# Kernel optimization log

Hardware: AMD Instinct MI355X
Metric: run time of the kernel (lower is better)

## Reference

```python
import jax, jax.numpy as jnp
import numpy as np

D_MODEL = 1024
D_STATE = 16
D_CONV = 4
BATCH = 2
SEQ = 2048


def setup_inputs() -> dict:
    key = jax.random.key(0)
    ks = jax.random.split(key, 10)
    s = lambda fan_in: 1.0 / np.sqrt(fan_in)
    x = jax.random.normal(ks[0], (BATCH, SEQ, D_MODEL), dtype=jnp.float32)
    W_in = jax.random.normal(ks[1], (D_MODEL, 2 * D_MODEL), dtype=jnp.float32) * s(D_MODEL)
    conv_w = jax.random.normal(ks[2], (D_MODEL, D_CONV), dtype=jnp.float32) * s(D_CONV)
    conv_b = jax.random.normal(ks[3], (D_MODEL,), dtype=jnp.float32) * 0.01
    W_x = jax.random.normal(ks[4], (D_MODEL, 2 * D_STATE), dtype=jnp.float32) * s(D_MODEL)
    W_dt = jax.random.normal(ks[5], (D_MODEL, D_MODEL), dtype=jnp.float32) * s(D_MODEL)
    b_dt = jax.random.normal(ks[6], (D_MODEL,), dtype=jnp.float32) * 0.01
    A_log = jax.random.normal(ks[7], (D_MODEL,), dtype=jnp.float32) * 0.1
    D_param = jnp.ones((D_MODEL,), dtype=jnp.float32)
    W_out = jax.random.normal(ks[8], (D_MODEL, D_MODEL), dtype=jnp.float32) * s(D_MODEL)
    return {"x": x, "W_in": W_in, "conv_w": conv_w, "conv_b": conv_b,
            "W_x": W_x, "W_dt": W_dt, "b_dt": b_dt, "A_log": A_log,
            "D_param": D_param, "W_out": W_out}


def _selective_scan(x, A, dt, B, C):
    # x, dt: [b, l, d]; A: [d]; B, C: [b, l, n]
    b, l, d = x.shape
    n = B.shape[-1]
    h0 = jnp.zeros((b, d, n), dtype=x.dtype)

    def step(h, inp):
        x_t, dt_t, B_t, C_t = inp  # [b,d], [b,d], [b,n], [b,n]
        dA = jnp.exp(dt_t * A)[..., None]            # [b, d, 1]
        h = h * dA + x_t[..., None] * B_t[:, None, :]  # [b, d, n]
        y_t = jnp.einsum('bdn,bn->bd', h, C_t)
        return h, y_t

    xs = (jnp.swapaxes(x, 0, 1), jnp.swapaxes(dt, 0, 1),
          jnp.swapaxes(B, 0, 1), jnp.swapaxes(C, 0, 1))
    _, ys = jax.lax.scan(step, h0, xs)               # ys: [l, b, d]
    return jnp.swapaxes(ys, 0, 1)


def _forward(x, W_in, conv_w, conv_b, W_x, W_dt, b_dt, A_log, D_param, W_out):
    seq_len = x.shape[1]
    xz = x @ W_in                                     # [b, l, 2d]
    x_ssm, z = jnp.split(xz, 2, axis=-1)
    # causal depthwise conv (torch pads both sides then slices -> left pad only)
    xc = jnp.swapaxes(x_ssm, 1, 2)                    # [b, d, l]
    kernel = conv_w[:, None, :]                       # [d, 1, k]
    xc = jax.lax.conv_general_dilated(
        xc, kernel, window_strides=(1,), padding=[(D_CONV - 1, 0)],
        dimension_numbers=('NCH', 'OIH', 'NCH'), feature_group_count=D_MODEL)
    xc = xc + conv_b[None, :, None]
    x_ssm = jnp.swapaxes(xc, 1, 2)[:, :seq_len]       # [b, l, d]
    x_ssm = jax.nn.silu(x_ssm)
    A = -jnp.exp(A_log)
    dt = jax.nn.softplus(x_ssm @ W_dt + b_dt)
    BC = x_ssm @ W_x
    B, C = jnp.split(BC, 2, axis=-1)
    y = _selective_scan(x_ssm, A, dt, B, C)
    y = y + x_ssm * D_param
    y = y * jax.nn.silu(z)
    return y @ W_out


def reference(x, W_in, conv_w, conv_b, W_x, W_dt, b_dt, A_log, D_param, W_out):
    return _forward(x, W_in, conv_w, conv_b, W_x, W_dt, b_dt, A_log, D_param, W_out)
```

## Files before the change

### kernel.cpp

```cpp
#include <hip/hip_runtime.h>
#include <hip/hip_bf16.h>
#include <math.h>

#define D_MODEL 1024
#define D_STATE 16
#define D_CONV  4
#define BATCH   2
#define SEQ     2048
#define MROWS   (BATCH * SEQ)
#define CHUNK   32
#define NCHUNK  (SEQ / CHUNK)
#define BD      (BATCH * D_MODEL)

typedef __attribute__((ext_vector_type(8))) short bf16x8;
typedef __attribute__((ext_vector_type(4))) float f32x4;

__device__ __forceinline__ unsigned short f2bf(float f) {
    unsigned int u = __builtin_bit_cast(unsigned int, f);
    u = (u + 0x7fffu + ((u >> 16) & 1u)) >> 16;
    return (unsigned short)u;
}
__device__ __forceinline__ float bf2f(unsigned short u) {
    return __builtin_bit_cast(float, (unsigned int)u << 16);
}
__device__ __forceinline__ float softplus_f(float v) {
    return (v > 20.f) ? v : log1pf(expf(v));
}

__device__ __forceinline__ void gl2lds16(const unsigned short* g, unsigned short* l) {
    __builtin_amdgcn_global_load_lds(
        (__attribute__((address_space(1))) void*)(void*)g,
        (__attribute__((address_space(3))) void*)(void*)l, 16, 0, 0);
}

__global__ __launch_bounds__(256) void prepass(
        const float* __restrict__ x, unsigned short* __restrict__ xb,
        const float* __restrict__ W_in, unsigned short* __restrict__ Wt_in,
        const float* __restrict__ W_dt, unsigned short* __restrict__ Wt_cat,
        const float* __restrict__ W_out, unsigned short* __restrict__ Wt_out,
        const float* __restrict__ Wx) {
    __shared__ float tile[32][33];
    const int blk = blockIdx.x;
    const int tid = threadIdx.x;

    if (blk < 2048) {
        const size_t i = ((size_t)blk * 256 + tid) * 8;
        const float4 v0 = *(const float4*)(x + i);
        const float4 v1 = *(const float4*)(x + i + 4);
        bf16x8 o;
        o[0] = (short)f2bf(v0.x); o[1] = (short)f2bf(v0.y);
        o[2] = (short)f2bf(v0.z); o[3] = (short)f2bf(v0.w);
        o[4] = (short)f2bf(v1.x); o[5] = (short)f2bf(v1.y);
        o[6] = (short)f2bf(v1.z); o[7] = (short)f2bf(v1.w);
        *(bf16x8*)(xb + i) = o;
        return;
    }
    if (blk < 2048 + 2048 + 1024 + 1024) {
        const float* W; unsigned short* Wt; int N, b;
        if (blk < 4096)      { W = W_in;  Wt = Wt_in;  N = 2048; b = blk - 2048; }
        else if (blk < 5120) { W = W_dt;  Wt = Wt_cat; N = 1024; b = blk - 4096; }
        else                 { W = W_out; Wt = Wt_out; N = 1024; b = blk - 5120; }
        const int nx = N / 32;
        const int n0 = (b % nx) * 32, k0 = (b / nx) * 32;
        const int tx = tid & 31, ty = tid >> 5;
#pragma unroll
        for (int r = 0; r < 4; ++r)
            tile[ty + r * 8][tx] = W[(size_t)(k0 + ty + r * 8) * N + n0 + tx];
        __syncthreads();
#pragma unroll
        for (int r = 0; r < 4; ++r)
            Wt[(size_t)(n0 + ty + r * 8) * 1024 + k0 + tx] = f2bf(tile[tx][ty + r * 8]);
        return;
    }
    {
        const int idx = (blk - 6144) * 256 + tid;
        const int k = idx & 1023;
        const int n = idx >> 10;
        unsigned short v = 0;
        if (n < 32) v = f2bf(Wx[(size_t)k * 32 + n]);
        Wt_cat[(size_t)(1024 + n) * 1024 + k] = v;
    }
}

template <int EPI>
__global__ __launch_bounds__(256) void gemm64(
        const unsigned short* __restrict__ A, const unsigned short* __restrict__ Bt,
        void* __restrict__ Cout, int N, int K,
        const float* __restrict__ bias, const float* __restrict__ alog,
        float* __restrict__ bc) {
    __shared__ unsigned short As[2][2 * 2048];
    __shared__ unsigned short Bs[2][2 * 4096];

    const int tid  = threadIdx.x;
    const int wave = tid >> 6, lane = tid & 63;
    const int q = lane >> 4, mr = lane & 15;
    const int m0 = blockIdx.y * 64, n0 = blockIdx.x * 128;

    f32x4 acc[4][2];
#pragma unroll
    for (int mi = 0; mi < 4; ++mi)
#pragma unroll
        for (int ni = 0; ni < 2; ++ni) acc[mi][ni] = {0.f, 0.f, 0.f, 0.f};

    const int kb = (tid & 3) * 8;
    const int rA = tid >> 2;
    const unsigned short* AgL = A + (size_t)(m0 + rA) * K + kb;
    const unsigned short* AgH = AgL + 32;
    const unsigned short* Bg0L = Bt + (size_t)(n0 + rA) * K + kb;
    const unsigned short* Bg0H = Bg0L + 32;
    const unsigned short* Bg1L = Bt + (size_t)(n0 + 64 + rA) * K + kb;
    const unsigned short* Bg1H = Bg1L + 32;
    const int sT = tid * 8;

    const int NK = K >> 6;
    gl2lds16(AgL, As[0] + sT);
    gl2lds16(AgH, As[0] + 2048 + sT);
    gl2lds16(Bg0L, Bs[0] + sT);
    gl2lds16(Bg1L, Bs[0] + 2048 + sT);
    gl2lds16(Bg0H, Bs[0] + 4096 + sT);
    gl2lds16(Bg1H, Bs[0] + 6144 + sT);

    for (int i = 0; i < NK; ++i) {
        __syncthreads();
        const int cur = i & 1, nxt = cur ^ 1;
        if (i + 1 < NK) {
            const int ko = (i + 1) * 64;
            gl2lds16(AgL + ko, As[nxt] + sT);
            gl2lds16(AgH + ko, As[nxt] + 2048 + sT);
            gl2lds16(Bg0L + ko, Bs[nxt] + sT);
            gl2lds16(Bg1L + ko, Bs[nxt] + 2048 + sT);
            gl2lds16(Bg0H + ko, Bs[nxt] + 4096 + sT);
            gl2lds16(Bg1H + ko, Bs[nxt] + 6144 + sT);
        }
#pragma unroll
        for (int ks = 0; ks < 2; ++ks) {
            bf16x8 af[4], bfr[2];
#pragma unroll
            for (int mi = 0; mi < 4; ++mi)
                af[mi] = *(const bf16x8*)(As[cur] + ks * 2048 + (mi * 16 + mr) * 32 + q * 8);
#pragma unroll
            for (int ni = 0; ni < 2; ++ni)
                bfr[ni] = *(const bf16x8*)(Bs[cur] + ks * 4096 +
                                           (wave * 32 + ni * 16 + mr) * 32 + q * 8);
#pragma unroll
            for (int mi = 0; mi < 4; ++mi)
#pragma unroll
                for (int ni = 0; ni < 2; ++ni)
                    acc[mi][ni] = __builtin_amdgcn_mfma_f32_16x16x32_bf16(
                        af[mi], bfr[ni], acc[mi][ni], 0, 0, 0);
        }
    }

#pragma unroll
    for (int ni = 0; ni < 2; ++ni) {
        const int col = n0 + wave * 32 + ni * 16 + mr;
        float be = 0.f, al = 0.f;
        if (EPI == 3 && col < 1024) { be = bias[col]; al = alog[col]; }
#pragma unroll
        for (int mi = 0; mi < 4; ++mi) {
            const int row0 = m0 + mi * 16 + q * 4;
#pragma unroll
            for (int r = 0; r < 4; ++r) {
                float v = acc[mi][ni][r];
                const int row = row0 + r;
                if (EPI == 0) {
                    ((float*)Cout)[(size_t)row * N + col] = v;
                } else if (EPI == 2) {
                    ((unsigned short*)Cout)[(size_t)row * N + col] = f2bf(v);
                } else {
                    if (col < 1024) {
                        float dt = softplus_f(v + be);
                        ((unsigned short*)Cout)[(size_t)row * 1024 + col] =
                            f2bf(expf(dt * (-expf(al))));
                    } else if (col < 1056) {
                        bc[(size_t)row * 32 + (col - 1024)] = v;
                    }
                }
            }
        }
    }
}

__global__ __launch_bounds__(256) void conv_silu_kernel(
        const unsigned short* __restrict__ xz, const float* __restrict__ conv_w,
        const float* __restrict__ conv_b, unsigned short* __restrict__ xssm) {
    const int idx = blockIdx.x * 256 + threadIdx.x;
    const int d8 = idx & 127;
    const int bt = idx >> 7;
    const int t  = bt & (SEQ - 1);
    const int d  = d8 * 8;

    float4 w[8];
#pragma unroll
    for (int i = 0; i < 8; ++i) w[i] = *(const float4*)&conv_w[(d + i) * 4];

    float acc[8];
    {
        const float4 b0 = *(const float4*)&conv_b[d];
        const float4 b1 = *(const float4*)&conv_b[d + 4];
        acc[0] = b0.x; acc[1] = b0.y; acc[2] = b0.z; acc[3] = b0.w;
        acc[4] = b1.x; acc[5] = b1.y; acc[6] = b1.z; acc[7] = b1.w;
    }

#pragma unroll
    for (int j = 0; j < D_CONV; ++j) {
        const int tt = t - (D_CONV - 1) + j;
        if (tt < 0) continue;
        const bf16x8 xv = *(const bf16x8*)(&xz[((size_t)(bt - t + tt)) * 2048 + d]);
        const float wj[8] = {j == 0 ? w[0].x : j == 1 ? w[0].y : j == 2 ? w[0].z : w[0].w,
                             j == 0 ? w[1].x : j == 1 ? w[1].y : j == 2 ? w[1].z : w[1].w,
                             j == 0 ? w[2].x : j == 1 ? w[2].y : j == 2 ? w[2].z : w[2].w,
                             j == 0 ? w[3].x : j == 1 ? w[3].y : j == 2 ? w[3].z : w[3].w,
                             j == 0 ? w[4].x : j == 1 ? w[4].y : j == 2 ? w[4].z : w[4].w,
                             j == 0 ? w[5].x : j == 1 ? w[5].y : j == 2 ? w[5].z : w[5].w,
                             j == 0 ? w[6].x : j == 1 ? w[6].y : j == 2 ? w[6].z : w[6].w,
                             j == 0 ? w[7].x : j == 1 ? w[7].y : j == 2 ? w[7].z : w[7].w};
#pragma unroll
        for (int i = 0; i < 8; ++i)
            acc[i] += bf2f((unsigned short)xv[i]) * wj[i];
    }
    bf16x8 o;
#pragma unroll
    for (int i = 0; i < 8; ++i) {
        const float s = acc[i] / (1.f + expf(-acc[i]));
        o[i] = (short)f2bf(s);
    }
    *(bf16x8*)(&xssm[(size_t)bt * D_MODEL + d]) = o;
}

__global__ __launch_bounds__(256) void scan_pass1(
        const unsigned short* __restrict__ xssm, const unsigned short* __restrict__ dA16,
        const float* __restrict__ BCb,
        float* __restrict__ Sbuf, float* __restrict__ Pbuf) {
    const int ch = blockIdx.x, dg = blockIdx.y, b = blockIdx.z;
    const int tid = threadIdx.x;
    const int dd  = dg * 256 + tid;
    const int t0  = ch * CHUNK;

    __shared__ float Bs[CHUNK][16];
    if (tid < CHUNK * 4) {
        const int t = tid >> 2, j = (tid & 3) * 4;
        *(float4*)&Bs[t][j] = *(const float4*)&BCb[((size_t)b * SEQ + t0 + t) * 32 + j];
    }
    __syncthreads();

    const size_t base = ((size_t)b * SEQ + t0) * D_MODEL + dd;
    float h[16];
#pragma unroll
    for (int n = 0; n < 16; ++n) h[n] = 0.f;
    float P = 1.f;

    for (int g = 0; g < CHUNK; g += 8) {
        float dAr[8], xr[8];
#pragma unroll
        for (int p = 0; p < 8; ++p) {
            const size_t o = base + (size_t)(g + p) * D_MODEL;
            dAr[p] = bf2f(dA16[o]);
            xr[p]  = bf2f(xssm[o]);
        }
#pragma unroll
        for (int p = 0; p < 8; ++p) {
            const int t = g + p;
            const float dA = dAr[p], x = xr[p];
            P *= dA;
            const float4 B0 = *(const float4*)&Bs[t][0];
            const float4 B1 = *(const float4*)&Bs[t][4];
            const float4 B2 = *(const float4*)&Bs[t][8];
            const float4 B3 = *(const float4*)&Bs[t][12];
            h[0]  = h[0]  * dA + x * B0.x;  h[1]  = h[1]  * dA + x * B0.y;
            h[2]  = h[2]  * dA + x * B0.z;  h[3]  = h[3]  * dA + x * B0.w;
            h[4]  = h[4]  * dA + x * B1.x;  h[5]  = h[5]  * dA + x * B1.y;
            h[6]  = h[6]  * dA + x * B1.z;  h[7]  = h[7]  * dA + x * B1.w;
            h[8]  = h[8]  * dA + x * B2.x;  h[9]  = h[9]  * dA + x * B2.y;
            h[10] = h[10] * dA + x * B2.z;  h[11] = h[11] * dA + x * B2.w;
            h[12] = h[12] * dA + x * B3.x;  h[13] = h[13] * dA + x * B3.y;
            h[14] = h[14] * dA + x * B3.z;  h[15] = h[15] * dA + x * B3.w;
        }
    }

    const int dn = b * D_MODEL + dd;
    const size_t so = ((size_t)ch * BD + dn) * 16;
#pragma unroll
    for (int n = 0; n < 16; n += 4)
        *(float4*)&Sbuf[so + n] = make_float4(h[n], h[n + 1], h[n + 2], h[n + 3]);
    Pbuf[(size_t)ch * BD + dn] = P;
}

__global__ __launch_bounds__(128) void scan_mid(
        const float* __restrict__ Sbuf, const float* __restrict__ Pbuf,
        float* __restrict__ Hin) {
    const int idx = blockIdx.x * 128 + threadIdx.x;
    const int n   = idx & 15;
    const int dn  = idx >> 4;

    float h = 0.f;
    for (int ch = 0; ch < NCHUNK; ++ch) {
        const size_t s = ((size_t)ch * BD + dn) * 16 + n;
        Hin[s] = h;
        h = Pbuf[(size_t)ch * BD + dn] * h + Sbuf[s];
    }
}

__global__ __launch_bounds__(256) void scan_pass2(
        const unsigned short* __restrict__ xssm, const unsigned short* __restrict__ dA16,
        const float* __restrict__ BCb, const unsigned short* __restrict__ xz,
        const float* __restrict__ Dp, const float* __restrict__ Hin,
        unsigned short* __restrict__ ybuf) {
    const int ch = blockIdx.x, dg = blockIdx.y, b = blockIdx.z;
    const int tid = threadIdx.x;
    const int dd  = dg * 256 + tid;
    const int t0  = ch * CHUNK;

    __shared__ float BCs[CHUNK][32];
    {
        const int t = tid >> 3, j = (tid & 7) * 4;
        *(float4*)&BCs[t][j] = *(const float4*)&BCb[((size_t)b * SEQ + t0 + t) * 32 + j];
    }
    __syncthreads();

    const float Dpv = Dp[dd];
    const size_t base  = ((size_t)b * SEQ + t0) * D_MODEL + dd;
    const size_t baseZ = ((size_t)b * SEQ + t0) * 2048 + D_MODEL + dd;

    float h[16];
    const int dn = b * D_MODEL + dd;
    const size_t ho = ((size_t)ch * BD + dn) * 16;
#pragma unroll
    for (int n = 0; n < 16; n += 4) {
        const float4 hv = *(const float4*)&Hin[ho + n];
        h[n] = hv.x; h[n + 1] = hv.y; h[n + 2] = hv.z; h[n + 3] = hv.w;
    }

    for (int g = 0; g < CHUNK; g += 8) {
        float dAr[8], xr[8], zr[8];
#pragma unroll
        for (int p = 0; p < 8; ++p) {
            const size_t o = base + (size_t)(g + p) * D_MODEL;
            dAr[p] = bf2f(dA16[o]);
            xr[p]  = bf2f(xssm[o]);
            zr[p]  = bf2f(xz[baseZ + (size_t)(g + p) * 2048]);
        }
#pragma unroll
        for (int p = 0; p < 8; ++p) {
            const int t = g + p;
            const float dA = dAr[p], x = xr[p];
            const float4 B0 = *(const float4*)&BCs[t][0];
            const float4 B1 = *(const float4*)&BCs[t][4];
            const float4 B2 = *(const float4*)&BCs[t][8];
            const float4 B3 = *(const float4*)&BCs[t][12];
            const float4 C0 = *(const float4*)&BCs[t][16];
            const float4 C1 = *(const float4*)&BCs[t][20];
            const float4 C2 = *(const float4*)&BCs[t][24];
            const float4 C3 = *(const float4*)&BCs[t][28];
            float y = 0.f;
            h[0]  = h[0]  * dA + x * B0.x;  y += h[0]  * C0.x;
            h[1]  = h[1]  * dA + x * B0.y;  y += h[1]  * C0.y;
            h[2]  = h[2]  * dA + x * B0.z;  y += h[2]  * C0.z;
            h[3]  = h[3]  * dA + x * B0.w;  y += h[3]  * C0.w;
            h[4]  = h[4]  * dA + x * B1.x;  y += h[4]  * C1.x;
            h[5]  = h[5]  * dA + x * B1.y;  y += h[5]  * C1.y;
            h[6]  = h[6]  * dA + x * B1.z;  y += h[6]  * C1.z;
            h[7]  = h[7]  * dA + x * B1.w;  y += h[7]  * C1.w;
            h[8]  = h[8]  * dA + x * B2.x;  y += h[8]  * C2.x;
            h[9]  = h[9]  * dA + x * B2.y;  y += h[9]  * C2.y;
            h[10] = h[10] * dA + x * B2.z;  y += h[10] * C2.z;
            h[11] = h[11] * dA + x * B2.w;  y += h[11] * C2.w;
            h[12] = h[12] * dA + x * B3.x;  y += h[12] * C3.x;
            h[13] = h[13] * dA + x * B3.y;  y += h[13] * C3.y;
            h[14] = h[14] * dA + x * B3.z;  y += h[14] * C3.z;
            h[15] = h[15] * dA + x * B3.w;  y += h[15] * C3.w;

            const float zv = zr[p];
            const float sz = zv / (1.f + expf(-zv));
            ybuf[base + (size_t)t * D_MODEL] = f2bf((y + x * Dpv) * sz);
        }
    }
}

extern "C" void kernel_launch(void* const* d_in, const int* in_sizes, int n_in,
                              void* d_out, int out_size, void* d_ws, size_t ws_size,
                              hipStream_t stream) {
    const float* x       = (const float*)d_in[0];
    const float* W_in    = (const float*)d_in[1];
    const float* conv_w  = (const float*)d_in[2];
    const float* conv_b  = (const float*)d_in[3];
    const float* W_x     = (const float*)d_in[4];
    const float* W_dt    = (const float*)d_in[5];
    const float* b_dt    = (const float*)d_in[6];
    const float* A_log   = (const float*)d_in[7];
    const float* D_param = (const float*)d_in[8];
    const float* W_out   = (const float*)d_in[9];
    float* out = (float*)d_out;
    char* ws   = (char*)d_ws;

    unsigned short* xz_bf   = (unsigned short*)(ws + 0);
    unsigned short* xssm_bf = (unsigned short*)(ws + 16777216);
    unsigned short* dAb16   = (unsigned short*)(ws + 25165824);
    float*          BCb     = (float*)(ws + 41943040);
    unsigned short* ybuf_bf = (unsigned short*)(ws + 42467328);
    unsigned short* xb      = (unsigned short*)(ws + 50855936);
    unsigned short* Wt_in   = (unsigned short*)(ws + 59244544);
    unsigned short* Wt_cat  = (unsigned short*)(ws + 63438848);
    unsigned short* Wt_out  = (unsigned short*)(ws + 65798144);
    float*          Sbuf    = (float*)(ws + 67895296);
    float*          Pbuf    = (float*)(ws + 76283904);
    float*          Hin     = (float*)(ws + 76808192);

    prepass<<<2048 + 2048 + 1024 + 1024 + 512, 256, 0, stream>>>(
        x, xb, W_in, Wt_in, W_dt, Wt_cat, W_out, Wt_out, W_x);

    gemm64<2><<<dim3(2048 / 128, MROWS / 64), 256, 0, stream>>>(
        xb, Wt_in, xz_bf, 2048, D_MODEL, nullptr, nullptr, nullptr);
    conv_silu_kernel<<<(MROWS * 128) / 256, 256, 0, stream>>>(xz_bf, conv_w, conv_b, xssm_bf);
    gemm64<3><<<dim3(1152 / 128, MROWS / 64), 256, 0, stream>>>(
        xssm_bf, Wt_cat, dAb16, 1152, D_MODEL, b_dt, A_log, BCb);
    scan_pass1<<<dim3(NCHUNK, D_MODEL / 256, BATCH), 256, 0, stream>>>(
        xssm_bf, dAb16, BCb, Sbuf, Pbuf);
    scan_mid<<<(BD * 16) / 128, 128, 0, stream>>>(Sbuf, Pbuf, Hin);
    scan_pass2<<<dim3(NCHUNK, D_MODEL / 256, BATCH), 256, 0, stream>>>(
        xssm_bf, dAb16, BCb, xz_bf, D_param, Hin, ybuf_bf);
    gemm64<0><<<dim3(1024 / 128, MROWS / 64), 256, 0, stream>>>(
        ybuf_bf, Wt_out, out, D_MODEL, D_MODEL, nullptr, nullptr, nullptr);
}
```

Baseline: 245.8 us.

## Replace direct global-to-LDS loads with register-staged prefetch and padded LDS rows

The GEMM tile loader stops using global_load_lds and instead loads two k-tiles ahead into registers, then writes them to LDS after the MFMA work for the current tile. The LDS layout changes from split 32-wide halves to padded rows of stride 68, meant to cut bank conflicts on fragment reads. A custom waitcnt+barrier replaces __syncthreads. This costs more registers and LDS per block, which may lower occupancy, and adds VGPR-to-LDS store instructions.

```diff
diff --git a/kernel.cpp b/kernel.cpp
--- a/kernel.cpp
+++ b/kernel.cpp
@@ -15,6 +15,8 @@
 typedef __attribute__((ext_vector_type(8))) short bf16x8;
 typedef __attribute__((ext_vector_type(4))) float f32x4;
 
+#define LSTRIDE 68
+
 __device__ __forceinline__ unsigned short f2bf(float f) {
     unsigned int u = __builtin_bit_cast(unsigned int, f);
     u = (u + 0x7fffu + ((u >> 16) & 1u)) >> 16;
@@ -27,10 +29,9 @@
     return (v > 20.f) ? v : log1pf(expf(v));
 }
 
-__device__ __forceinline__ void gl2lds16(const unsigned short* g, unsigned short* l) {
-    __builtin_amdgcn_global_load_lds(
-        (__attribute__((address_space(1))) void*)(void*)g,
-        (__attribute__((address_space(3))) void*)(void*)l, 16, 0, 0);
+__device__ __forceinline__ void lds_barrier() {
+    __builtin_amdgcn_s_waitcnt(0xc07f);
+    __builtin_amdgcn_s_barrier();
 }
 
 __global__ __launch_bounds__(256) void prepass(
@@ -88,8 +89,8 @@
         void* __restrict__ Cout, int N, int K,
         const float* __restrict__ bias, const float* __restrict__ alog,
         float* __restrict__ bc) {
-    __shared__ unsigned short As[2][2 * 2048];
-    __shared__ unsigned short Bs[2][2 * 4096];
+    __shared__ unsigned short As[2][64 * LSTRIDE];
+    __shared__ unsigned short Bs[2][128 * LSTRIDE];
 
     const int tid  = threadIdx.x;
     const int wave = tid >> 6, lane = tid & 63;
@@ -103,51 +104,71 @@
         for (int ni = 0; ni < 2; ++ni) acc[mi][ni] = {0.f, 0.f, 0.f, 0.f};
 
     const int kb = (tid & 3) * 8;
-    const int rA = tid >> 2;
-    const unsigned short* AgL = A + (size_t)(m0 + rA) * K + kb;
-    const unsigned short* AgH = AgL + 32;
-    const unsigned short* Bg0L = Bt + (size_t)(n0 + rA) * K + kb;
-    const unsigned short* Bg0H = Bg0L + 32;
-    const unsigned short* Bg1L = Bt + (size_t)(n0 + 64 + rA) * K + kb;
-    const unsigned short* Bg1H = Bg1L + 32;
-    const int sT = tid * 8;
+    const int rT = tid >> 2;
+    const unsigned short* Ag  = A + (size_t)(m0 + rT) * K + kb;
+    const unsigned short* Bg0 = Bt + (size_t)(n0 + rT) * K + kb;
+    const unsigned short* Bg1 = Bt + (size_t)(n0 + 64 + rT) * K + kb;
+    const int aOff  = rT * LSTRIDE + kb;
+    const int b0Off = rT * LSTRIDE + kb;
+    const int b1Off = (64 + rT) * LSTRIDE + kb;
 
     const int NK = K >> 6;
-    gl2lds16(AgL, As[0] + sT);
-    gl2lds16(AgH, As[0] + 2048 + sT);
-    gl2lds16(Bg0L, Bs[0] + sT);
-    gl2lds16(Bg1L, Bs[0] + 2048 + sT);
-    gl2lds16(Bg0H, Bs[0] + 4096 + sT);
-    gl2lds16(Bg1H, Bs[0] + 6144 + sT);
+    bf16x8 R[2][6];
+#pragma unroll
+    for (int p = 0; p < 2; ++p) {
+        const int ko = p * 64;
+        R[p][0] = *(const bf16x8*)(Ag + ko);
+        R[p][1] = *(const bf16x8*)(Ag + ko + 32);
+        R[p][2] = *(const bf16x8*)(Bg0 + ko);
+        R[p][3] = *(const bf16x8*)(Bg0 + ko + 32);
+        R[p][4] = *(const bf16x8*)(Bg1 + ko);
+        R[p][5] = *(const bf16x8*)(Bg1 + ko + 32);
+    }
+    *(bf16x8*)(As[0] + aOff)       = R[0][0];
+    *(bf16x8*)(As[0] + aOff + 32)  = R[0][1];
+    *(bf16x8*)(Bs[0] + b0Off)      = R[0][2];
+    *(bf16x8*)(Bs[0] + b0Off + 32) = R[0][3];
+    *(bf16x8*)(Bs[0] + b1Off)      = R[0][4];
+    *(bf16x8*)(Bs[0] + b1Off + 32) = R[0][5];
+    lds_barrier();
 
     for (int i = 0; i < NK; ++i) {
-        __syncthreads();
         const int cur = i & 1, nxt = cur ^ 1;
-        if (i + 1 < NK) {
-            const int ko = (i + 1) * 64;
-            gl2lds16(AgL + ko, As[nxt] + sT);
-            gl2lds16(AgH + ko, As[nxt] + 2048 + sT);
-            gl2lds16(Bg0L + ko, Bs[nxt] + sT);
-            gl2lds16(Bg1L + ko, Bs[nxt] + 2048 + sT);
-            gl2lds16(Bg0H + ko, Bs[nxt] + 4096 + sT);
-            gl2lds16(Bg1H + ko, Bs[nxt] + 6144 + sT);
+        if (i + 2 < NK) {
+            const int ko = (i + 2) * 64;
+            R[cur][0] = *(const bf16x8*)(Ag + ko);
+            R[cur][1] = *(const bf16x8*)(Ag + ko + 32);
+            R[cur][2] = *(const bf16x8*)(Bg0 + ko);
+            R[cur][3] = *(const bf16x8*)(Bg0 + ko + 32);
+            R[cur][4] = *(const bf16x8*)(Bg1 + ko);
+            R[cur][5] = *(const bf16x8*)(Bg1 + ko + 32);
         }
 #pragma unroll
         for (int ks = 0; ks < 2; ++ks) {
             bf16x8 af[4], bfr[2];
 #pragma unroll
             for (int mi = 0; mi < 4; ++mi)
-                af[mi] = *(const bf16x8*)(As[cur] + ks * 2048 + (mi * 16 + mr) * 32 + q * 8);
+                af[mi] = *(const bf16x8*)(As[cur] + (mi * 16 + mr) * LSTRIDE +
+                                          ks * 32 + q * 8);
 #pragma unroll
             for (int ni = 0; ni < 2; ++ni)
-                bfr[ni] = *(const bf16x8*)(Bs[cur] + ks * 4096 +
-                                           (wave * 32 + ni * 16 + mr) * 32 + q * 8);
+                bfr[ni] = *(const bf16x8*)(Bs[cur] + (wave * 32 + ni * 16 + mr) * LSTRIDE +
+                                           ks * 32 + q * 8);
 #pragma unroll
             for (int mi = 0; mi < 4; ++mi)
 #pragma unroll
                 for (int ni = 0; ni < 2; ++ni)
                     acc[mi][ni] = __builtin_amdgcn_mfma_f32_16x16x32_bf16(
                         af[mi], bfr[ni], acc[mi][ni], 0, 0, 0);
+        }
+        if (i + 1 < NK) {
+            *(bf16x8*)(As[nxt] + aOff)       = R[nxt][0];
+            *(bf16x8*)(As[nxt] + aOff + 32)  = R[nxt][1];
+            *(bf16x8*)(Bs[nxt] + b0Off)      = R[nxt][2];
+            *(bf16x8*)(Bs[nxt] + b0Off + 32) = R[nxt][3];
+            *(bf16x8*)(Bs[nxt] + b1Off)      = R[nxt][4];
+            *(bf16x8*)(Bs[nxt] + b1Off + 32) = R[nxt][5];
+            lds_barrier();
         }
     }
 
```

After: 423.1 us. 72.1% more time.
